# Optimization experiments

Hardware: AMD Instinct MI355X
Metric: run time of the kernel (lower is better)

Reference implementation:

```python
import jax, jax.numpy as jnp
import numpy as np

IN_F = 135; D = 512; K = 10; DCT_N = 34; IN_N = 120; OUT_N = 24
VL = K + OUT_N          # 34, window length
VN = IN_N - K - OUT_N + 1  # 87, number of windows
NSTAGE = 2
BN_SCALE = 1.0 / np.sqrt(1.0 + 1e-5)  # eval-mode BN with default running stats (mean 0, var 1)


def get_dct_matrix(N):
    dct_m = np.eye(N)
    for k in range(N):
        for i in range(N):
            w = np.sqrt(2.0 / N)
            if k == 0:
                w = np.sqrt(1.0 / N)
            dct_m[k, i] = w * np.cos(np.pi * (i + 0.5) * k / N)
    idct_m = np.linalg.inv(dct_m)
    return dct_m, idct_m

_DCT_NP, _IDCT_NP = get_dct_matrix(VL)
DCT = jnp.asarray(_DCT_NP[:DCT_N], dtype=jnp.float32)        # [34,34] (dct_n == vl)
IDCT = jnp.asarray(_IDCT_NP[:, :DCT_N], dtype=jnp.float32)   # [34,34]

WIN_IDX = np.arange(VL)[None, :] + np.arange(VN)[:, None]    # [87,34]
PAD_IDX = np.concatenate([np.arange(IN_N - K, IN_N), np.full(OUT_N, IN_N - 1)])  # last 10 frames + last frame repeated


def conv1d(x, w):
    return jax.lax.conv_general_dilated(x, w, (1,), 'VALID',
                                        dimension_numbers=('NCH', 'OIH', 'NCH'))


def gconv(x, att, w, b):
    # GraphConvolution: att @ (x @ w) + b ; x: [b,n,f_in]
    return jnp.einsum('nm,bmf->bnf', att, x @ w) + b


def bn_eval(y, g, b):
    bs, n, f = y.shape
    v = y.reshape(bs, n * f)
    v = g * (v * BN_SCALE) + b
    return v.reshape(bs, n, f)


def setup_inputs() -> dict:
    key = jax.random.key(0)
    ks = jax.random.split(key, 20)
    s = 0.05  # small init scale so tanh/att stay in sane range
    return {
        'poses':    jax.random.normal(ks[0], (256, 144, 135), jnp.float32),
        'qw1':      jax.random.normal(ks[1], (512, 135, 6)) * s,
        'qw2':      jax.random.normal(ks[2], (512, 512, 5)) * s,
        'kw1':      jax.random.normal(ks[3], (512, 135, 6)) * s,
        'kw2':      jax.random.normal(ks[4], (512, 512, 5)) * s,
        'gc1_att':  jax.random.normal(ks[5], (135, 135)) * s,
        'gc1_w':    jax.random.normal(ks[6], (68, 512)) * s,
        'gc1_b':    jax.random.normal(ks[7], (512,)) * s,
        'bn1_g':    jnp.ones((69120,), jnp.float32),
        'bn1_b':    jnp.zeros((69120,), jnp.float32),
        'gcb_att':  jax.random.normal(ks[8], (4, 135, 135)) * s,
        'gcb_w':    jax.random.normal(ks[9], (4, 512, 512)) * s,
        'gcb_b':    jax.random.normal(ks[10], (4, 512)) * s,
        'gcb_g':    jnp.ones((4, 69120), jnp.float32),
        'gcb_beta': jnp.zeros((4, 69120), jnp.float32),
        'gc7_att':  jax.random.normal(ks[11], (135, 135)) * s,
        'gc7_w':    jax.random.normal(ks[12], (512, 68)) * s,
        'gc7_b':    jax.random.normal(ks[13], (68,)) * s,
    }


def reference(poses, qw1, qw2, kw1, kw2,
              gc1_att, gc1_w, gc1_b, bn1_g, bn1_b,
              gcb_att, gcb_w, gcb_b, gcb_g, gcb_beta,
              gc7_att, gc7_w, gc7_b):
    src = poses[:, :IN_N]                      # [b,120,135]
    bs = src.shape[0]
    src_t = jnp.transpose(src, (0, 2, 1))      # [b,135,120]
    key_in = src_t[:, :, :IN_N - OUT_N] / 1000.0   # [b,135,96]
    qry_in = src_t[:, :, -K:] / 1000.0             # [b,135,10]

    key_f = jax.nn.relu(conv1d(jax.nn.relu(conv1d(key_in, kw1)), kw2))  # [b,512,87]
    qry_f = jax.nn.relu(conv1d(jax.nn.relu(conv1d(qry_in, qw1)), qw2))  # [b,512,1]

    # non-softmax attention: matmul + eps-normalize
    score = jnp.einsum('bdq,bdk->bqk', qry_f, key_f) + 1e-15   # [b,1,87]
    att = score / jnp.sum(score, axis=2, keepdims=True)

    # overlapping windows -> DCT of each window
    windows = src[:, WIN_IDX]                                   # [b,87,34,135]
    val = jnp.einsum('kt,bvtf->bvfk', DCT, windows).reshape(bs, VN, IN_F * DCT_N)
    dct_att = jnp.einsum('bqv,bvz->bqz', att, val)[:, 0].reshape(bs, IN_F, DCT_N)

    input_gcn = src[:, PAD_IDX]                                 # [b,34,135]
    dct_in = jnp.einsum('kt,btf->bfk', DCT, input_gcn)          # [b,135,34]
    x = jnp.concatenate([dct_in, dct_att], axis=-1)             # [b,135,68]

    # GCN (eval mode: dropout = identity, BN uses running stats)
    y = jnp.tanh(bn_eval(gconv(x, gc1_att, gc1_w, gc1_b), bn1_g, bn1_b))
    for i in range(NSTAGE):
        res = y
        h = jnp.tanh(bn_eval(gconv(y, gcb_att[2 * i], gcb_w[2 * i], gcb_b[2 * i]),
                             gcb_g[2 * i], gcb_beta[2 * i]))
        h = jnp.tanh(bn_eval(gconv(h, gcb_att[2 * i + 1], gcb_w[2 * i + 1], gcb_b[2 * i + 1]),
                             gcb_g[2 * i + 1], gcb_beta[2 * i + 1]))
        y = h + res
    y = gconv(y, gc7_att, gc7_w, gc7_b) + x                     # [b,135,68]

    out = jnp.einsum('tk,bfk->btf', IDCT, y[:, :, :DCT_N])      # [b,34,135]
    preds = out[:, -OUT_N:, :]                                  # [b,24,135]
    return preds
```

## Files before the change

kernel.cpp:

```cpp
#include <hip/hip_runtime.h>
#include <math.h>

#define POSE_ROWS 144
#define NF 135
#define DD 512
#define KQ 10
#define DCTN 34
#define INN 120
#define OUTN 24
#define VN 87
#define BATCH 256
#define RP 34816
#define NODEP 136
#define BN_SCALE 0.9999950000374997f

typedef __attribute__((ext_vector_type(8))) short short8;
typedef __attribute__((ext_vector_type(4))) float floatx4;

static __device__ __forceinline__ ushort f2bf(float f) {
    unsigned u = __builtin_bit_cast(unsigned, f);
    u = (u + 0x7FFFu + ((u >> 16) & 1u)) >> 16;
    return (ushort)u;
}
static __device__ __forceinline__ float bf2f(ushort s) {
    return __builtin_bit_cast(float, (unsigned)s << 16);
}
static __device__ __forceinline__ float tanh_fast(float x) {
    float ax = __builtin_fabsf(x);
    float e = __builtin_amdgcn_exp2f(ax * -2.885390081777927f);
    float t = (1.f - e) * __builtin_amdgcn_rcpf(1.f + e);
    return __builtin_copysignf(t, x);
}

#define GLOAD_LDS(gp, lp) __builtin_amdgcn_global_load_lds( \
    (const __attribute__((address_space(1))) unsigned int*)(const void*)(gp), \
    (__attribute__((address_space(3))) unsigned int*)(void*)(lp), 16, 0, 0)

#define PB_POSES 19584
#define PB_K1B   22912
#define PB_K2B   33152
#define PB_WT1   33408
#define PB_WTB   37504
#define PB_WT7   37640
#define PB_A1    37742
#define PB_AB    38147
#define PB_A7    38249
#define PB_BN    39609
#define PB_Z     39610
#define PB_DCT   39615

__global__ __launch_bounds__(256) void prep_all(
    const float* __restrict__ poses, ushort* __restrict__ pb16,
    const float* __restrict__ kw1, const float* __restrict__ qw1,
    ushort* __restrict__ Wt1k, ushort* __restrict__ Wt1q,
    const float* __restrict__ kw2, const float* __restrict__ qw2,
    ushort* __restrict__ Wt2k, ushort* __restrict__ Wt2q,
    const float* __restrict__ gc1_w, ushort* __restrict__ WT1,
    const float* __restrict__ gcb_w, ushort* __restrict__ WTb,
    const float* __restrict__ gc7_w, ushort* __restrict__ WT7,
    const float* __restrict__ gc1_att, ushort* __restrict__ A16_1,
    const float* __restrict__ gcb_att, ushort* __restrict__ A16_B,
    const float* __restrict__ gc7_att, ushort* __restrict__ A16_7,
    const float* __restrict__ bn1_g, const float* __restrict__ bn1_b,
    const float* __restrict__ gcb_g, const float* __restrict__ gcb_beta,
    float* __restrict__ bnT, float* __restrict__ zpadf, float* __restrict__ dct)
{
    const int blk = blockIdx.x;
    const int tid = threadIdx.x;
    if (blk < PB_POSES) {
        int idx = blk * 256 + tid;
        int i = idx % NODEP;
        int row = (idx / NODEP) % POSE_ROWS;
        int b = idx / (NODEP * POSE_ROWS);
        float v = (i < NF) ? poses[((long long)b * POSE_ROWS + row) * NF + i] * 1e-3f : 0.f;
        pb16[idx] = f2bf(v);
    } else if (blk < PB_K1B) {
        int wi = blk - PB_POSES;
        const float* src = (wi < 1664) ? kw1 : qw1;
        ushort* dst = (wi < 1664) ? Wt1k : Wt1q;
        int idx = (wi % 1664) * 256 + tid;
        int n = idx / 832, k = idx % 832;
        int h = k / 136, i = k % 136;
        float v = (i < 135 && h < 6) ? src[((long long)n * 135 + i) * 6 + h] : 0.f;
        dst[idx] = f2bf(v);
    } else if (blk < PB_K2B) {
        int wi = blk - PB_K1B;
        const float* src = (wi < 5120) ? kw2 : qw2;
        ushort* dst = (wi < 5120) ? Wt2k : Wt2q;
        int idx = (wi % 5120) * 256 + tid;
        int n = idx / 2560, k = idx % 2560;
        int h = k / 512, i = k % 512;
        dst[idx] = f2bf(src[((long long)n * 512 + i) * 5 + h]);
    } else if (blk < PB_WT1) {
        int idx = (blk - PB_K2B) * 256 + tid;
        int n = idx / 128, k = idx % 128;
        WT1[idx] = f2bf((k < 68) ? gc1_w[(long long)k * 512 + n] : 0.f);
    } else if (blk < PB_WTB) {
        int g = (blk - PB_WT1) * 256 + tid;
        int L = g >> 18, idx = g & 262143;
        int n = idx / 512, k = idx % 512;
        WTb[g] = f2bf(gcb_w[(long long)L * 262144 + (long long)k * 512 + n]);
    } else if (blk < PB_WT7) {
        int idx = (blk - PB_WTB) * 256 + tid;
        int n = idx / 512, k = idx % 512;
        WT7[idx] = f2bf(gc7_w[(long long)k * 68 + n]);
    } else if (blk < PB_A1) {
        int idx = (blk - PB_WT7) * 256 + tid;
        if (idx < 135 * 192) {
            int r = idx / 192, c = idx % 192;
            A16_1[idx] = f2bf(c < 135 ? gc1_att[r * 135 + c] : 0.f);
        }
    } else if (blk < PB_AB) {
        int idx = (blk - PB_A1) * 256 + tid;
        int r = idx / 192, c = idx % 192;
        A16_B[idx] = f2bf(c < 135 ? gcb_att[r * 135 + c] : 0.f);
    } else if (blk < PB_A7) {
        int idx = (blk - PB_AB) * 256 + tid;
        if (idx < 135 * 192) {
            int r = idx / 192, c = idx % 192;
            A16_7[idx] = f2bf(c < 135 ? gc7_att[r * 135 + c] : 0.f);
        }
    } else if (blk < PB_BN) {
        int g = (blk - PB_A7) * 256 + tid;
        int p = g / 69632, idx = g % 69632;
        int node = idx % 136, m = idx / 136;
        const float* gs = (p == 0) ? bn1_g : (gcb_g + (p - 1) * 69120);
        const float* bs = (p == 0) ? bn1_b : (gcb_beta + (p - 1) * 69120);
        float* gt = bnT + (long long)p * 139264;
        float* bt = gt + 69632;
        gt[idx] = (node < 135) ? gs[node * 512 + m] : 0.f;
        bt[idx] = (node < 135) ? bs[node * 512 + m] : 0.f;
    } else if (blk < PB_Z) {
        if (tid < 128) zpadf[tid] = 0.f;
    } else {
        int idx = (blk - PB_Z) * 256 + tid;
        if (idx < DCTN * DCTN) {
            int k = idx / DCTN, i = idx % DCTN;
            double w = (k == 0) ? sqrt(1.0 / DCTN) : sqrt(2.0 / DCTN);
            dct[idx] = (float)(w * cos(3.14159265358979323846 * (i + 0.5) * k / (double)DCTN));
        }
    }
}

template<int BM, int BN>
__global__ __launch_bounds__(256) void gemm2(
    const ushort* __restrict__ A, const ushort* __restrict__ Bt,
    const ushort* __restrict__ zpad,
    int M, int N, int K,
    int mode, int CNT, int Pc,
    int rpbA, long long sAw, long long sAr, long long sAbz,
    long long sBr, long long sBbz,
    float* __restrict__ C, ushort* __restrict__ C16,
    long long sCbz, long long sCm, long long sCn,
    int do_relu, const float* __restrict__ bias, int bias_mode,
    const float* __restrict__ bnTg, const float* __restrict__ bnTb,
    int do_tanh, const ushort* __restrict__ resid16, const float* __restrict__ resid32)
{
    constexpr int SM = BM / 32, SN = BN / 32;
    constexpr int RA = BM / 32, RB = BN / 32;
    __shared__ ushort As[BM * 64];
    __shared__ ushort Bs[BN * 64];

    int mb, nb;
    if (mode == 0) { mb = blockIdx.y; nb = blockIdx.x; }
    else {
        int gx = blockIdx.x;
        int x = gx & 7, s = gx >> 3;
        if (mode == 1) { mb = s % CNT; nb = x * Pc + s / CNT; }
        else           { nb = s % CNT; mb = x * Pc + s / CNT; }
    }
    const int m0 = mb * BM, n0 = nb * BN;
    if (m0 >= M || n0 >= N) return;

    const int tid = threadIdx.x;
    const int lane = tid & 63, w = tid >> 6;
    const int bz = blockIdx.z;
    const int wm = (w >> 1) * (BM / 2), wn = (w & 1) * (BN / 2);
    const int chunk = (lane & 7) ^ ((lane >> 3) & 7);

    const ushort* pA[RA]; int stA[RA];
    #pragma unroll
    for (int j = 0; j < RA; j++) {
        int m = m0 + j * 32 + w * 8 + (lane >> 3);
        bool v = m < M;
        long long off = v ? ((long long)(m / rpbA) * sAw + (long long)(m % rpbA) * sAr
                            + (long long)bz * sAbz) : 0;
        pA[j] = v ? (A + off + chunk * 8) : (zpad + chunk * 8);
        stA[j] = v ? 64 : 0;
    }
    const ushort* pB[RB]; int stB[RB];
    #pragma unroll
    for (int j = 0; j < RB; j++) {
        int n = n0 + j * 32 + w * 8 + (lane >> 3);
        bool v = n < N;
        long long off = v ? ((long long)n * sBr + (long long)bz * sBbz) : 0;
        pB[j] = v ? (Bt + off + chunk * 8) : (zpad + chunk * 8);
        stB[j] = v ? 64 : 0;
    }

    floatx4 acc[SM][SN];
    #pragma unroll
    for (int i = 0; i < SM; i++)
        #pragma unroll
        for (int j = 0; j < SN; j++)
            acc[i][j] = (floatx4){0.f, 0.f, 0.f, 0.f};

    for (int k0 = 0; k0 < K; k0 += 64) {
        #pragma unroll
        for (int j = 0; j < RA; j++)
            GLOAD_LDS(pA[j], &As[(j * 32 + w * 8) * 64]);
        #pragma unroll
        for (int j = 0; j < RB; j++)
            GLOAD_LDS(pB[j], &Bs[(j * 32 + w * 8) * 64]);
        __syncthreads();

        #pragma unroll
        for (int kk = 0; kk < 2; kk++) {
            short8 af[SM], bf[SN];
            #pragma unroll
            for (int sm = 0; sm < SM; sm++) {
                int lr = wm + sm * 16 + (lane & 15);
                int slot = ((lane >> 4) + kk * 4) ^ (lr & 7);
                af[sm] = *(const short8*)&As[lr * 64 + slot * 8];
            }
            #pragma unroll
            for (int sn = 0; sn < SN; sn++) {
                int lr = wn + sn * 16 + (lane & 15);
                int slot = ((lane >> 4) + kk * 4) ^ (lr & 7);
                bf[sn] = *(const short8*)&Bs[lr * 64 + slot * 8];
            }
            #pragma unroll
            for (int sm = 0; sm < SM; sm++)
                #pragma unroll
                for (int sn = 0; sn < SN; sn++)
                    acc[sm][sn] = __builtin_amdgcn_mfma_f32_16x16x32_bf16(af[sm], bf[sn], acc[sm][sn], 0, 0, 0);
        }
        __syncthreads();

        #pragma unroll
        for (int j = 0; j < RA; j++) pA[j] += stA[j];
        #pragma unroll
        for (int j = 0; j < RB; j++) pB[j] += stB[j];
    }

    const int lc = lane & 15;
    const int lr4 = (lane >> 4) << 2;
    #pragma unroll
    for (int sm = 0; sm < SM; sm++) {
        #pragma unroll
        for (int sn = 0; sn < SN; sn++) {
            int n = n0 + wn + sn * 16 + lc;
            if (n >= N) continue;
            int node = n % 136;
            int mbv = m0 + wm + sm * 16 + lr4;
            float vv[4];
            #pragma unroll
            for (int r = 0; r < 4; r++) {
                int m = mbv + r;
                float v = acc[sm][sn][r];
                if (do_relu) v = fmaxf(v, 0.f);
                if (bias) v += (bias_mode == 1) ? bias[m < M ? m : 0] : bias[n];
                if (bnTg) {
                    long long gi = (long long)(m < M ? m : 0) * 136 + node;
                    v = bnTg[gi] * (v * BN_SCALE) + bnTb[gi];
                }
                if (do_tanh) v = tanh_fast(v);
                long long addr = (long long)bz * sCbz + (long long)m * sCm + (long long)n * sCn;
                if (m < M) {
                    if (resid16) v += bf2f(resid16[addr]);
                    else if (resid32) v += resid32[addr];
                    if (C) C[addr] = v;
                    if (C16 && sCm != 1) C16[addr] = f2bf(v);
                }
                vv[r] = v;
            }
            if (C16 && sCm == 1 && mbv + 3 < M) {
                ushort4 pk;
                pk.x = f2bf(vv[0]); pk.y = f2bf(vv[1]); pk.z = f2bf(vv[2]); pk.w = f2bf(vv[3]);
                *(ushort4*)&C16[(long long)bz * sCbz + mbv + (long long)n * sCn] = pk;
            }
        }
    }
}

__global__ __launch_bounds__(512, 2) void fused_layer(
    const ushort* __restrict__ Yin,
    const ushort* __restrict__ Att,
    const ushort* __restrict__ Wt,
    const ushort* __restrict__ zpad,
    const float* __restrict__ bias,
    const float* __restrict__ bnTg, const float* __restrict__ bnTb,
    const ushort* __restrict__ resid16,
    ushort* __restrict__ Yout)
{
    extern __shared__ ushort zs[];
    const int b = blockIdx.x;
    const int tid = threadIdx.x;
    const int lane = tid & 63, w = tid >> 6;
    const int ln = lane & 15;
    const int lk8 = (lane >> 4) * 8;
    const int lr4 = (lane >> 4) << 2;
    const long long ybase = (long long)b * 136;

    {
        const int cp = w * 64;
        const ushort* pb[9];
        #pragma unroll
        for (int nt = 0; nt < 9; nt++) {
            int n = nt * 16 + ln;
            pb[nt] = (n < 135) ? (Att + (long long)n * 192 + lk8) : (zpad + lk8);
        }
        const ushort* pa[4];
        #pragma unroll
        for (int sm = 0; sm < 4; sm++) {
            int c = cp + sm * 16 + ln;
            pa[sm] = Yin + (long long)c * RP + ybase + lk8;
        }
        floatx4 acc[4][9];
        #pragma unroll
        for (int i = 0; i < 4; i++)
            #pragma unroll
            for (int j = 0; j < 9; j++)
                acc[i][j] = (floatx4){0.f, 0.f, 0.f, 0.f};

        #pragma unroll
        for (int kc = 0; kc < 3; kc++) {
            #pragma unroll
            for (int kk = 0; kk < 2; kk++) {
                if (kc == 2 && kk == 1) continue;
                const int ko = kc * 64 + kk * 32;
                short8 af[4], bf[9];
                #pragma unroll
                for (int sm = 0; sm < 4; sm++)
                    af[sm] = *(const short8*)(pa[sm] + ko);
                #pragma unroll
                for (int nt = 0; nt < 9; nt++)
                    bf[nt] = *(const short8*)(pb[nt] + ko);
                #pragma unroll
                for (int sm = 0; sm < 4; sm++)
                    #pragma unroll
                    for (int nt = 0; nt < 9; nt++)
                        acc[sm][nt] = __builtin_amdgcn_mfma_f32_16x16x32_bf16(af[sm], bf[nt], acc[sm][nt], 0, 0, 0);
            }
        }
        #pragma unroll
        for (int sm = 0; sm < 4; sm++) {
            #pragma unroll
            for (int nt = 0; nt < 9; nt++) {
                int n = nt * 16 + ln;
                if (n >= 136) continue;
                int c = cp + sm * 16 + lr4;
                ushort4 pk;
                pk.x = f2bf(acc[sm][nt][0]);
                pk.y = f2bf(acc[sm][nt][1]);
                pk.z = f2bf(acc[sm][nt][2]);
                pk.w = f2bf(acc[sm][nt][3]);
                int chs = (c >> 3) ^ (n & 7);
                *(ushort4*)&zs[n * 512 + chs * 8 + (c & 7)] = pk;
            }
        }
    }
    __syncthreads();

    {
        const int p = (w >> 1) * 128;
        const int nt0 = (w & 1) ? 4 : 0;
        const ushort* pw[8];
        #pragma unroll
        for (int sm = 0; sm < 8; sm++)
            pw[sm] = Wt + (long long)(p + sm * 16 + ln) * 512 + lk8;
        int zrow[5], zx[5];
        #pragma unroll
        for (int j = 0; j < 5; j++) {
            int n = (nt0 + j) * 16 + ln;
            int nn = (n < 136) ? n : 0;
            zrow[j] = nn * 512;
            zx[j] = nn & 7;
        }
        floatx4 acc[8][5];
        #pragma unroll
        for (int i = 0; i < 8; i++)
            #pragma unroll
            for (int j = 0; j < 5; j++)
                acc[i][j] = (floatx4){0.f, 0.f, 0.f, 0.f};

        #pragma unroll
        for (int kc = 0; kc < 8; kc++) {
            #pragma unroll
            for (int kk = 0; kk < 2; kk++) {
                const int ko = kc * 64 + kk * 32;
                const int kchunk = kc * 8 + kk * 4 + (lane >> 4);
                short8 af[8], bf[5];
                #pragma unroll
                for (int sm = 0; sm < 8; sm++)
                    af[sm] = *(const short8*)(pw[sm] + ko);
                #pragma unroll
                for (int j = 0; j < 5; j++)
                    bf[j] = *(const short8*)&zs[zrow[j] + (kchunk ^ zx[j]) * 8];
                #pragma unroll
                for (int sm = 0; sm < 8; sm++)
                    #pragma unroll
                    for (int j = 0; j < 5; j++)
                        acc[sm][j] = __builtin_amdgcn_mfma_f32_16x16x32_bf16(af[sm], bf[j], acc[sm][j], 0, 0, 0);
            }
        }
        #pragma unroll
        for (int sm = 0; sm < 8; sm++) {
            #pragma unroll
            for (int j = 0; j < 5; j++) {
                int nt = nt0 + j;
                if (nt == 4 && (w & 1) == 0) continue;
                int n = nt * 16 + ln;
                if (n >= 136) continue;
                int c2 = p + sm * 16 + lr4;
                #pragma unroll
                for (int r = 0; r < 4; r++) {
                    int m = c2 + r;
                    float v = acc[sm][j][r];
                    v += bias[m];
                    long long gi = (long long)m * 136 + n;
                    v = bnTg[gi] * (v * BN_SCALE) + bnTb[gi];
                    v = tanh_fast(v);
                    long long addr = (long long)m * RP + ybase + n;
                    if (resid16) v += bf2f(resid16[addr]);
                    Yout[addr] = f2bf(v);
                }
            }
        }
    }
}

__global__ __launch_bounds__(256) void att_k(const float* __restrict__ kf, const float* __restrict__ qf,
                                             float* __restrict__ att) {
    int b = blockIdx.x;
    int tid = threadIdx.x;
    int lane = tid & 63, w = tid >> 6;
    __shared__ float s[96];
    __shared__ float ssum;
    const float* qb = qf + b * DD + lane * 8;
    float4 q0 = *(const float4*)qb;
    float4 q1 = *(const float4*)(qb + 4);
    const float* kb = kf + (long long)b * VN * DD;
    for (int v = w; v < VN; v += 4) {
        const float* kr = kb + v * DD + lane * 8;
        float4 k0 = *(const float4*)kr;
        float4 k1 = *(const float4*)(kr + 4);
        float p = q0.x * k0.x + q0.y * k0.y + q0.z * k0.z + q0.w * k0.w
                + q1.x * k1.x + q1.y * k1.y + q1.z * k1.z + q1.w * k1.w;
        #pragma unroll
        for (int off = 32; off; off >>= 1) p += __shfl_xor(p, off);
        if (lane == 0) s[v] = p + 1e-15f;
    }
    __syncthreads();
    if (tid < 64) {
        float p2 = (tid < VN ? s[tid] : 0.f) + ((tid + 64) < VN ? s[tid + 64] : 0.f);
        #pragma unroll
        for (int off = 32; off; off >>= 1) p2 += __shfl_xor(p2, off);
        if (tid == 0) ssum = p2;
    }
    __syncthreads();
    float inv = 1.f / ssum;
    for (int v = tid; v < VN; v += 256) att[b * VN + v] = s[v] * inv;
}

__global__ void weighted_k(const float* __restrict__ poses, const float* __restrict__ att,
                           float* __restrict__ w34) {
    int t = blockIdx.x;
    int b = blockIdx.y;
    int f = threadIdx.x;
    if (f >= NF) return;
    const float* pb = poses + (long long)b * POSE_ROWS * NF + t * NF + f;
    const float* ab = att + b * VN;
    float acc = 0.f;
    for (int v = 0; v < VN; v++) acc += ab[v] * pb[v * NF];
    w34[(long long)b * DCTN * NF + t * NF + f] = acc;
}

__global__ void build_x(const float* __restrict__ poses, const float* __restrict__ w34,
                        const float* __restrict__ dctm, float* __restrict__ x32,
                        ushort* __restrict__ xT16) {
    int idx = blockIdx.x * 256 + threadIdx.x;
    if (idx >= BATCH * NF * 68) return;
    int kk = idx % 68;
    int f = (idx / 68) % NF;
    int b = idx / (68 * NF);
    float acc = 0.f;
    if (kk < DCTN) {
        const float* pb = poses + (long long)b * POSE_ROWS * NF;
        #pragma unroll
        for (int t = 0; t < DCTN; t++) {
            int row = (t < KQ) ? (INN - KQ + t) : (INN - 1);
            acc += dctm[kk * DCTN + t] * pb[row * NF + f];
        }
    } else {
        int k2 = kk - DCTN;
        const float* wb = w34 + (long long)b * DCTN * NF + f;
        #pragma unroll
        for (int t = 0; t < DCTN; t++) acc += dctm[k2 * DCTN + t] * wb[t * NF];
    }
    long long R = (long long)b * NODEP + f;
    x32[R * 68 + kk] = acc;
    xT16[(long long)kk * RP + R] = f2bf(acc);
}

__global__ void idct_out(const float* __restrict__ h32, const float* __restrict__ dctm,
                         float* __restrict__ out) {
    int idx = blockIdx.x * 256 + threadIdx.x;
    if (idx >= BATCH * OUTN * NF) return;
    int f = idx % NF;
    int t = (idx / NF) % OUTN;
    int b = idx / (NF * OUTN);
    const float* yr = h32 + ((long long)b * NODEP + f) * 68;
    float acc = 0.f;
    #pragma unroll
    for (int k = 0; k < DCTN; k++) acc += dctm[k * DCTN + (KQ + t)] * yr[k];
    out[idx] = acc;
}

extern "C" void kernel_launch(void* const* d_in, const int* in_sizes, int n_in,
                              void* d_out, int out_size, void* d_ws, size_t ws_size,
                              hipStream_t stream) {
    const float* poses   = (const float*)d_in[0];
    const float* qw1     = (const float*)d_in[1];
    const float* qw2     = (const float*)d_in[2];
    const float* kw1     = (const float*)d_in[3];
    const float* kw2     = (const float*)d_in[4];
    const float* gc1_att = (const float*)d_in[5];
    const float* gc1_w   = (const float*)d_in[6];
    const float* gc1_b   = (const float*)d_in[7];
    const float* bn1_g   = (const float*)d_in[8];
    const float* bn1_b   = (const float*)d_in[9];
    const float* gcb_att = (const float*)d_in[10];
    const float* gcb_w   = (const float*)d_in[11];
    const float* gcb_b   = (const float*)d_in[12];
    const float* gcb_g   = (const float*)d_in[13];
    const float* gcb_beta= (const float*)d_in[14];
    const float* gc7_att = (const float*)d_in[15];
    const float* gc7_w   = (const float*)d_in[16];
    const float* gc7_b   = (const float*)d_in[17];
    float* out = (float*)d_out;
    float* w = (float*)d_ws;

    float* dct   = w;
    float* att   = w + 1280;
    float* w34   = w + 23808;
    float* x32   = w + 1198848;
    float* h32   = w + 3566336;
    float* qf    = w + 5933824;
    ushort* su   = (ushort*)(w + 6064896);
    ushort* WT1    = su;
    ushort* WTb    = su + 65536;
    ushort* WT7    = su + 1114112;
    ushort* A16_1  = su + 1148928;
    ushort* A16_B  = su + 1174848;
    ushort* A16_7  = su + 1278528;
    float* bnT   = w + 6717120;
    float* kf    = w + 7413440;
    ushort* R2   = (ushort*)(w + 18816704);
    ushort* yT16  = R2;
    ushort* r1k16 = R2;
    ushort* r1q16 = R2 + 11927552;
    ushort* R3   = (ushort*)(w + 27729600);
    ushort* hT16  = R3;
    ushort* pb16  = R3;
    ushort* Wt1k  = R3 + 5013504;
    ushort* Wt1q  = R3 + 5439488;
    ushort* Wt2k  = R3 + 5865472;
    ushort* Wt2q  = R3 + 7176192;
    ushort* R4   = (ushort*)(w + 36642496);
    ushort* zN16  = R4;
    ushort* xT16  = R4;
    ushort* z116  = R4 + 2367488;
    float* zpadf = w + 45555392;
    const ushort* zpad = (const ushort*)zpadf;

    const int INF_RPB = 1 << 30;

    static int lds_set = 0;
    if (!lds_set) {
        hipFuncSetAttribute((const void*)fused_layer,
                            hipFuncAttributeMaxDynamicSharedMemorySize, 139264);
        lds_set = 1;
    }

    prep_all<<<PB_DCT, 256, 0, stream>>>(
        poses, pb16, kw1, qw1, Wt1k, Wt1q, kw2, qw2, Wt2k, Wt2q,
        gc1_w, WT1, gcb_w, WTb, gc7_w, WT7,
        gc1_att, A16_1, gcb_att, A16_B, gc7_att, A16_7,
        bn1_g, bn1_b, gcb_g, gcb_beta, bnT, zpadf, dct);

    gemm2<128,64><<<dim3(1472, 1, 1), 256, 0, stream>>>(pb16, Wt1k, zpad, 23296, 512, 832,
        2, 8, 23, 91, 19584LL, 136LL, 0LL, 832LL, 0LL,
        (float*)nullptr, r1k16, 0LL, 512LL, 1LL, 1, nullptr, 0, nullptr, nullptr, 0, nullptr, nullptr);
    gemm2<128,128><<<dim3(4, 10, 1), 256, 0, stream>>>(pb16 + 110*136, Wt1q, zpad, 1280, 512, 832,
        0, 0, 0, 5, 19584LL, 136LL, 0LL, 832LL, 0LL,
        (float*)nullptr, r1q16, 0LL, 512LL, 1LL, 1, nullptr, 0, nullptr, nullptr, 0, nullptr, nullptr);
    gemm2<128,64><<<dim3(1408, 1, 1), 256, 0, stream>>>(r1k16, Wt2k, zpad, 22272, 512, 2560,
        2, 8, 22, 87, 46592LL, 512LL, 0LL, 2560LL, 0LL,
        kf, (ushort*)nullptr, 0LL, 512LL, 1LL, 1, nullptr, 0, nullptr, nullptr, 0, nullptr, nullptr);
    gemm2<64,64><<<dim3(8, 4, 1), 256, 0, stream>>>(r1q16, Wt2q, zpad, 256, 512, 2560,
        0, 0, 0, INF_RPB, 0LL, 2560LL, 0LL, 2560LL, 0LL,
        qf, (ushort*)nullptr, 0LL, 512LL, 1LL, 1, nullptr, 0, nullptr, nullptr, 0, nullptr, nullptr);

    att_k<<<BATCH, 256, 0, stream>>>(kf, qf, att);
    weighted_k<<<dim3(DCTN, BATCH), 192, 0, stream>>>(poses, att, w34);
    build_x<<<(BATCH * NF * 68 + 255) / 256, 256, 0, stream>>>(poses, w34, dct, x32, xT16);

    gemm2<64,64><<<dim3(3, 2, BATCH), 256, 0, stream>>>(xT16, A16_1, zpad, 68, 135, 192,
        0, 0, 0, INF_RPB, 0LL, (long long)RP, 136LL, 192LL, 0LL,
        (float*)nullptr, z116, 10880LL, 1LL, 80LL, 0, nullptr, 0, nullptr, nullptr, 0, nullptr, nullptr);
    gemm2<128,64><<<dim3(2176, 1, 1), 256, 0, stream>>>(WT1, z116, zpad, 512, RP, 128,
        1, 4, 68, INF_RPB, 0LL, 128LL, 0LL, 80LL, 0LL,
        (float*)nullptr, yT16, 0LL, (long long)RP, 1LL, 0, gc1_b, 1, bnT, bnT + 69632, 1, nullptr, nullptr);

    for (int L = 0; L < 4; L++) {
        const ushort* min = (L & 1) ? hT16 : yT16;
        ushort* mout = (L & 1) ? yT16 : hT16;
        fused_layer<<<dim3(BATCH, 1, 1), 512, 139264, stream>>>(
            min, A16_B + L * 25920, WTb + L * 262144, zpad,
            gcb_b + L * 512, bnT + (1 + L) * 139264, bnT + (1 + L) * 139264 + 69632,
            (L & 1) ? yT16 : (const ushort*)nullptr, mout);
    }

    gemm2<64,64><<<dim3(3, 8, BATCH), 256, 0, stream>>>(yT16, A16_7, zpad, 512, 135, 192,
        0, 0, 0, INF_RPB, 0LL, (long long)RP, 136LL, 192LL, 0LL,
        (float*)nullptr, zN16, 69632LL, 1LL, 512LL, 0, nullptr, 0, nullptr, nullptr, 0, nullptr, nullptr);
    gemm2<64,64><<<dim3(1088, 1, 1), 256, 0, stream>>>(zN16, WT7, zpad, RP, 68, 512,
        2, 2, 68, INF_RPB, 0LL, 512LL, 0LL, 512LL, 0LL,
        h32, (ushort*)nullptr, 0LL, 68LL, 1LL, 0, gc7_b, 2, nullptr, nullptr, 0, nullptr, x32);

    idct_out<<<(BATCH * OUTN * NF + 255) / 256, 256, 0, stream>>>(h32, dct, out);
}
```

Measured before the change: 1.019 ms.

## Retile fused_layer second GEMM to 64-channel warp tiles and drop min-blocks bound

Changes the second GEMM's warp tiling from 128 channels by 5 node tiles (8x5 accumulators) to 64 channels by all 9 node tiles (4x9), matching the first GEMM's tiling. Both GEMM loops now load one B fragment at a time inside the node loop instead of holding arrays of fragments. The launch bound drops the min-2-blocks hint, which lets the compiler use more registers. The aim is to cut register pressure and spilling and remove the load imbalance of the 5-tile split, at the cost of possibly lower occupancy and more LDS reads per MFMA in the second GEMM.

```diff
diff --git a/kernel.cpp b/kernel.cpp
--- a/kernel.cpp
+++ b/kernel.cpp
@@ -283,7 +283,7 @@
     }
 }
 
-__global__ __launch_bounds__(512, 2) void fused_layer(
+__global__ __launch_bounds__(512) void fused_layer(
     const ushort* __restrict__ Yin,
     const ushort* __restrict__ Att,
     const ushort* __restrict__ Wt,
@@ -301,9 +301,9 @@
     const int lk8 = (lane >> 4) * 8;
     const int lr4 = (lane >> 4) << 2;
     const long long ybase = (long long)b * 136;
+    const int cp = w * 64;
 
     {
-        const int cp = w * 64;
         const ushort* pb[9];
         #pragma unroll
         for (int nt = 0; nt < 9; nt++) {
@@ -324,23 +324,18 @@
                 acc[i][j] = (floatx4){0.f, 0.f, 0.f, 0.f};
 
         #pragma unroll
-        for (int kc = 0; kc < 3; kc++) {
-            #pragma unroll
-            for (int kk = 0; kk < 2; kk++) {
-                if (kc == 2 && kk == 1) continue;
-                const int ko = kc * 64 + kk * 32;
-                short8 af[4], bf[9];
+        for (int ks = 0; ks < 5; ks++) {
+            const int ko = ks * 32;
+            short8 af[4];
+            #pragma unroll
+            for (int sm = 0; sm < 4; sm++)
+                af[sm] = *(const short8*)(pa[sm] + ko);
+            #pragma unroll
+            for (int nt = 0; nt < 9; nt++) {
+                short8 bfv = *(const short8*)(pb[nt] + ko);
                 #pragma unroll
                 for (int sm = 0; sm < 4; sm++)
-                    af[sm] = *(const short8*)(pa[sm] + ko);
-                #pragma unroll
-                for (int nt = 0; nt < 9; nt++)
-                    bf[nt] = *(const short8*)(pb[nt] + ko);
-                #pragma unroll
-                for (int sm = 0; sm < 4; sm++)
-                    #pragma unroll
-                    for (int nt = 0; nt < 9; nt++)
-                        acc[sm][nt] = __builtin_amdgcn_mfma_f32_16x16x32_bf16(af[sm], bf[nt], acc[sm][nt], 0, 0, 0);
+                    acc[sm][nt] = __builtin_amdgcn_mfma_f32_16x16x32_bf16(af[sm], bfv, acc[sm][nt], 0, 0, 0);
             }
         }
         #pragma unroll
@@ -363,60 +358,52 @@
     __syncthreads();
 
     {
-        const int p = (w >> 1) * 128;
-        const int nt0 = (w & 1) ? 4 : 0;
-        const ushort* pw[8];
-        #pragma unroll
-        for (int sm = 0; sm < 8; sm++)
-            pw[sm] = Wt + (long long)(p + sm * 16 + ln) * 512 + lk8;
-        int zrow[5], zx[5];
-        #pragma unroll
-        for (int j = 0; j < 5; j++) {
-            int n = (nt0 + j) * 16 + ln;
+        const ushort* pw[4];
+        #pragma unroll
+        for (int sm = 0; sm < 4; sm++)
+            pw[sm] = Wt + (long long)(cp + sm * 16 + ln) * 512 + lk8;
+        int zrow[9], zx[9];
+        #pragma unroll
+        for (int nt = 0; nt < 9; nt++) {
+            int n = nt * 16 + ln;
             int nn = (n < 136) ? n : 0;
-            zrow[j] = nn * 512;
-            zx[j] = nn & 7;
-        }
-        floatx4 acc[8][5];
-        #pragma unroll
-        for (int i = 0; i < 8; i++)
-            #pragma unroll
-            for (int j = 0; j < 5; j++)
+            zrow[nt] = nn * 512;
+            zx[nt] = nn & 7;
+        }
+        floatx4 acc[4][9];
+        #pragma unroll
+        for (int i = 0; i < 4; i++)
+            #pragma unroll
+            for (int j = 0; j < 9; j++)
                 acc[i][j] = (floatx4){0.f, 0.f, 0.f, 0.f};
 
         #pragma unroll
-        for (int kc = 0; kc < 8; kc++) {
-            #pragma unroll
-            for (int kk = 0; kk < 2; kk++) {
-                const int ko = kc * 64 + kk * 32;
-                const int kchunk = kc * 8 + kk * 4 + (lane >> 4);
-                short8 af[8], bf[5];
+        for (int ks = 0; ks < 16; ks++) {
+            const int ko = ks * 32;
+            const int kchunk = ks * 4 + (lane >> 4);
+            short8 af[4];
+            #pragma unroll
+            for (int sm = 0; sm < 4; sm++)
+                af[sm] = *(const short8*)(pw[sm] + ko);
+            #pragma unroll
+            for (int nt = 0; nt < 9; nt++) {
+                short8 bfv = *(const short8*)&zs[zrow[nt] + (kchunk ^ zx[nt]) * 8];
                 #pragma unroll
-                for (int sm = 0; sm < 8; sm++)
-                    af[sm] = *(const short8*)(pw[sm] + ko);
-                #pragma unroll
-                for (int j = 0; j < 5; j++)
-                    bf[j] = *(const short8*)&zs[zrow[j] + (kchunk ^ zx[j]) * 8];
-                #pragma unroll
-                for (int sm = 0; sm < 8; sm++)
-                    #pragma unroll
-                    for (int j = 0; j < 5; j++)
-                        acc[sm][j] = __builtin_amdgcn_mfma_f32_16x16x32_bf16(af[sm], bf[j], acc[sm][j], 0, 0, 0);
-            }
-        }
-        #pragma unroll
-        for (int sm = 0; sm < 8; sm++) {
-            #pragma unroll
-            for (int j = 0; j < 5; j++) {
-                int nt = nt0 + j;
-                if (nt == 4 && (w & 1) == 0) continue;
+                for (int sm = 0; sm < 4; sm++)
+                    acc[sm][nt] = __builtin_amdgcn_mfma_f32_16x16x32_bf16(af[sm], bfv, acc[sm][nt], 0, 0, 0);
+            }
+        }
+        #pragma unroll
+        for (int sm = 0; sm < 4; sm++) {
+            #pragma unroll
+            for (int nt = 0; nt < 9; nt++) {
                 int n = nt * 16 + ln;
                 if (n >= 136) continue;
-                int c2 = p + sm * 16 + lr4;
+                int c2 = cp + sm * 16 + lr4;
                 #pragma unroll
                 for (int r = 0; r < 4; r++) {
                     int m = c2 + r;
-                    float v = acc[sm][j][r];
+                    float v = acc[sm][nt][r];
                     v += bias[m];
                     long long gi = (long long)m * 136 + n;
                     v = bnTg[gi] * (v * BN_SCALE) + bnTb[gi];
```

Measured after the change: 895.7 us. 1.14x faster.
